# Kernel tuning notes

Measured on AMD Instinct MI355X. Metric: run time of the kernel, lower is better.

The kernel has to match this reference:

```python
import jax, jax.numpy as jnp
import numpy as np

B, N, NODE_DIM, D, H, K, VP = 64, 1024, 8, 128, 4, 16, 128
FF = 512


def _layernorm(x, g, b):
    m = jnp.mean(x, axis=-1, keepdims=True)
    v = jnp.var(x, axis=-1, keepdims=True)
    return (x - m) * jax.lax.rsqrt(v + 1e-5) * g + b


def setup_inputs() -> dict:
    key = jax.random.key(0)
    kit = iter(jax.random.split(key, 64))

    def w(*shape):
        fan_in = shape[-2] if len(shape) >= 2 else shape[-1]
        return jax.random.normal(next(kit), shape, jnp.float32) / np.sqrt(fan_in)

    return dict(
        node_inputs=jax.random.normal(next(kit), (B, N, NODE_DIM), jnp.float32),
        node_padding_mask=jnp.zeros((B, 1, N), jnp.bool_),
        current_index=jax.random.randint(next(kit), (B, 1, 1), 0, N),
        viewpoints=jax.random.randint(next(kit), (B, VP, 1), 0, N),
        viewpoint_padding_mask=jnp.zeros((B, 1, VP), jnp.bool_),
        adj_list=jax.random.randint(next(kit), (B, N, K), 0, N),
        W_init=w(NODE_DIM, D), b_init=jnp.zeros((D,), jnp.float32),
        gcn_W=w(4, D, D), gcn_b=jnp.zeros((4, D), jnp.float32),
        tc_fc_W=w(D, D), tc_fc_b=jnp.zeros((D,), jnp.float32),
        tc_ln1_g=jnp.ones((D,), jnp.float32), tc_ln1_b=jnp.zeros((D,), jnp.float32),
        Wq=w(D, H * D), bq=jnp.zeros((H * D,), jnp.float32),
        Wk=w(D, H * D), bk=jnp.zeros((H * D,), jnp.float32),
        Wv=w(D, H * D), bv=jnp.zeros((H * D,), jnp.float32),
        tc_ln2_g=jnp.ones((D,), jnp.float32), tc_ln2_b=jnp.zeros((D,), jnp.float32),
        sg_fc_W=w(D, D), sg_fc_b=jnp.zeros((D,), jnp.float32),
        dec_Wq=w(D, D), dec_Wk=w(D, D), dec_Wv=w(D, D), dec_Wo=w(D, D),
        dec_ln1_g=jnp.ones((D,), jnp.float32), dec_ln1_b=jnp.zeros((D,), jnp.float32),
        ff_W1=w(D, FF), ff_b1=jnp.zeros((FF,), jnp.float32),
        ff_W2=w(FF, D), ff_b2=jnp.zeros((D,), jnp.float32),
        dec_ln2_g=jnp.ones((D,), jnp.float32), dec_ln2_b=jnp.zeros((D,), jnp.float32),
        q_W=w(3 * D, 1), q_b=jnp.zeros((1,), jnp.float32),
    )


def _forward(node_inputs, node_padding_mask, current_index, viewpoints, viewpoint_padding_mask, adj_list,
             W_init, b_init, gcn_W, gcn_b, tc_fc_W, tc_fc_b, tc_ln1_g, tc_ln1_b,
             Wq, bq, Wk, bk, Wv, bv, tc_ln2_g, tc_ln2_b, sg_fc_W, sg_fc_b,
             dec_Wq, dec_Wk, dec_Wv, dec_Wo, dec_ln1_g, dec_ln1_b,
             ff_W1, ff_b1, ff_W2, ff_b2, dec_ln2_g, dec_ln2_b, q_W, q_b):
    Bb, Nn, nd = node_inputs.shape
    d = W_init.shape[1]
    nH = Wq.shape[1] // d  # SGFormer attention heads (per-head dim = d)
    BN = Bb * Nn
    # ---- initial embedding + batched block-diagonal sparse edges (prepare_batch_data) ----
    x0 = node_inputs.reshape(BN, nd) @ W_init + b_init
    offset = (jnp.arange(Bb) * Nn)[:, None, None]
    valid = adj_list >= 0
    row = (jnp.broadcast_to(jnp.arange(Nn)[None, :, None], adj_list.shape) + offset).reshape(-1)
    col = (jnp.where(valid, adj_list, 0) + offset).reshape(-1)
    ew = valid.reshape(-1).astype(x0.dtype)
    deg = jax.ops.segment_sum(ew, row, num_segments=BN) + 1.0  # +1 self-loop
    dinv = jax.lax.rsqrt(deg)
    enorm = (dinv[row] * dinv[col] * ew)[:, None]

    def gcn_conv(h, W, b):
        hw = h @ W
        agg = jax.ops.segment_sum(enorm * hw[col], row, num_segments=BN)
        return agg + hw / deg[:, None] + b  # self-loop term D^-1 * x W

    h = x0
    n_layers = gcn_W.shape[0]
    for i in range(n_layers):
        h = gcn_conv(h, gcn_W[i], gcn_b[i])
        if i < n_layers - 1:
            h = jax.nn.relu(h)
    gnn_out = h
    # ---- SGFormer TransConv: fc -> LN -> relu, then linear global attention over all BN nodes ----
    z0 = jax.nn.relu(_layernorm(x0 @ tc_fc_W + tc_fc_b, tc_ln1_g, tc_ln1_b))
    q = (z0 @ Wq + bq).reshape(BN, nH, d)
    k = (z0 @ Wk + bk).reshape(BN, nH, d)
    v = (z0 @ Wv + bv).reshape(BN, nH, d)
    qs = q / jnp.linalg.norm(q)  # global Frobenius norm, as in SGFormer
    ks = k / jnp.linalg.norm(k)
    Nf = jnp.asarray(BN, x0.dtype)
    kvs = jnp.einsum('lhm,lhd->hmd', ks, v)
    num = jnp.einsum('nhm,hmd->nhd', qs, kvs) + Nf * v
    den = jnp.einsum('nhm,hm->nh', qs, ks.sum(axis=0))[..., None] + Nf
    attn = (num / den).mean(axis=1)  # mean over heads -> [BN, d]
    z = jax.nn.relu(_layernorm(0.5 * attn + 0.5 * z0, tc_ln2_g, tc_ln2_b))  # alpha=0.5 residual
    enhanced = ((0.8 * gnn_out + 0.2 * z) @ sg_fc_W + sg_fc_b).reshape(Bb, Nn, d)  # graph_weight=0.8
    # ---- decoder: gather current node, masked cross-attention to all nodes ----
    cur = jnp.take_along_axis(enhanced, jnp.broadcast_to(current_index, (Bb, 1, d)), axis=1)
    dH = 4
    dk = d // dH
    qd = (cur @ dec_Wq).reshape(Bb, 1, dH, dk).transpose(0, 2, 1, 3)
    kd = (enhanced @ dec_Wk).reshape(Bb, Nn, dH, dk).transpose(0, 2, 1, 3)
    vd = (enhanced @ dec_Wv).reshape(Bb, Nn, dH, dk).transpose(0, 2, 1, 3)
    scores = jnp.einsum('bhqe,bhne->bhqn', qd, kd) / np.sqrt(dk).astype(np.float32)
    scores = jnp.where(node_padding_mask[:, None, :, :], -1e9, scores)
    wts = jax.nn.softmax(scores, axis=-1)
    att = jnp.einsum('bhqn,bhne->bhqe', wts, vd).transpose(0, 2, 1, 3).reshape(Bb, 1, d) @ dec_Wo
    t = _layernorm(cur + att, dec_ln1_g, dec_ln1_b)
    glob = _layernorm(t + jax.nn.relu(t @ ff_W1 + ff_b1) @ ff_W2 + ff_b2, dec_ln2_g, dec_ln2_b)
    # ---- Q head: gather viewpoints, concat(global, current, viewpoint) -> Linear(3d, 1) ----
    Vp = viewpoints.shape[1]
    vp = jnp.take_along_axis(enhanced, jnp.broadcast_to(viewpoints, (Bb, Vp, d)), axis=1)
    cs = jnp.concatenate([glob, cur], axis=-1)  # [B,1,2d]
    af = jnp.concatenate([jnp.broadcast_to(cs, (Bb, Vp, 2 * d)), vp], axis=-1)
    return af @ q_W + q_b  # [B, Vp, 1]


def reference(node_inputs, node_padding_mask, current_index, viewpoints, viewpoint_padding_mask, adj_list,
              W_init, b_init, gcn_W, gcn_b, tc_fc_W, tc_fc_b, tc_ln1_g, tc_ln1_b,
              Wq, bq, Wk, bk, Wv, bv, tc_ln2_g, tc_ln2_b, sg_fc_W, sg_fc_b,
              dec_Wq, dec_Wk, dec_Wv, dec_Wo, dec_ln1_g, dec_ln1_b,
              ff_W1, ff_b1, ff_W2, ff_b2, dec_ln2_g, dec_ln2_b, q_W, q_b):
    return _forward(node_inputs, node_padding_mask, current_index, viewpoints, viewpoint_padding_mask, adj_list,
                    W_init, b_init, gcn_W, gcn_b, tc_fc_W, tc_fc_b, tc_ln1_g, tc_ln1_b,
                    Wq, bq, Wk, bk, Wv, bv, tc_ln2_g, tc_ln2_b, sg_fc_W, sg_fc_b,
                    dec_Wq, dec_Wk, dec_Wv, dec_Wo, dec_ln1_g, dec_ln1_b,
                    ff_W1, ff_b1, ff_W2, ff_b2, dec_ln2_g, dec_ln2_b, q_W, q_b)
```

## Files before the change

### kernel.cpp

```cpp
#include <hip/hip_runtime.h>

#define BNn 65536L

typedef unsigned short u16;
typedef unsigned int u32;
typedef __attribute__((ext_vector_type(8))) short short8;
typedef __attribute__((ext_vector_type(4))) float f32x4;

__device__ inline u16 f2b(float f){ u32 u = __float_as_uint(f); u32 r = (u + 0x7fffu + ((u>>16)&1u))>>16; return (u16)r; }
__device__ inline float b2f(u16 b){ return __uint_as_float(((u32)b)<<16); }

__global__ __launch_bounds__(256) void k_init(const float* __restrict__ gcnW, const float* __restrict__ tcW,
                       const float* __restrict__ sgW, const float* __restrict__ dKW,
                       const float* __restrict__ dVW,
                       const float* __restrict__ Wq, const float* __restrict__ Wk, const float* __restrict__ Wv,
                       const float* __restrict__ in, const float* __restrict__ Wi, const float* __restrict__ bi,
                       const int* __restrict__ adj, float* __restrict__ dinv,
                       u16* __restrict__ wts, float* __restrict__ SqSkz, u16* __restrict__ x0) {
  __shared__ u16 sT[64 * 136];
  __shared__ float Ws[1024];
  __shared__ float bs[128];
  __shared__ float ins[256];
  int bid = blockIdx.x, t = threadIdx.x;
  if (bid < 41) {
    if (bid == 40) {
      if (t < 130) SqSkz[t] = 0.0f;
      return;
    }
    const float* src; long dst; int lds_src;
    if (bid < 16) {
      int mtx = bid >> 1, kh = bid & 1;
      src = (mtx < 4 ? gcnW + mtx * 16384 : mtx == 4 ? tcW : mtx == 5 ? sgW : mtx == 6 ? dKW : dVW) + kh * 64 * 128;
      dst = (long)mtx * 16384 + kh * 64;
      lds_src = 128;
    } else {
      int q = bid - 16; int mat = q >> 3, rem = q & 7, kh = rem >> 2, cb = rem & 3;
      src = (mat == 0 ? Wq : mat == 1 ? Wk : Wv) + kh * 64 * 512 + cb * 128;
      dst = 131072L + (long)(mat * 512 + cb * 128) * 128 + kh * 64;
      lds_src = 512;
    }
#pragma unroll
    for (int i = 0; i < 32; i++) {
      int idx = t + i * 256; int row = idx >> 7, col = idx & 127;
      sT[row * 136 + col] = f2b(src[(long)row * lds_src + col]);
    }
    __syncthreads();
    {
      int n = t >> 1, kb = t & 1;
      u16 ob[32];
#pragma unroll
      for (int k = 0; k < 32; k++) ob[k] = sT[(kb * 32 + k) * 136 + n];
      uint4* o4 = (uint4*)(wts + dst + (long)n * 128 + kb * 32);
      uint4* s4 = (uint4*)ob;
#pragma unroll
      for (int k = 0; k < 4; k++) o4[k] = s4[k];
    }
    return;
  }
  int b = bid - 41;
  long row0 = (long)b * 32;
  if (b < 256) {
    int n = b * 256 + t;
    int cnt = 0;
#pragma unroll
    for (int j = 0; j < 16; j++) cnt += (adj[(long)n * 16 + j] >= 0) ? 1 : 0;
    dinv[n] = rsqrtf((float)cnt + 1.0f);
  }
#pragma unroll
  for (int i = 0; i < 4; i++) Ws[t + i * 256] = Wi[t + i * 256];
  if (t < 128) bs[t] = bi[t];
  ins[t] = in[row0 * 8 + t];
  __syncthreads();
  int row = t >> 3, seg = t & 7;
  float acc[16];
#pragma unroll
  for (int i = 0; i < 16; i++) acc[i] = bs[seg * 16 + i];
#pragma unroll
  for (int k = 0; k < 8; k++) {
    float f = ins[row * 8 + k];
#pragma unroll
    for (int i = 0; i < 16; i++) acc[i] += f * Ws[k * 128 + seg * 16 + i];
  }
  u16 ob[16];
#pragma unroll
  for (int i = 0; i < 16; i++) ob[i] = f2b(acc[i]);
  uint4* o4 = (uint4*)(x0 + (row0 + row) * 128 + seg * 16);
  uint4* s4 = (uint4*)ob;
  o4[0] = s4[0]; o4[1] = s4[1];
}

template<int EPI>
__global__ __launch_bounds__(256) void k_gemm(const u16* __restrict__ A,
                                              const u16* __restrict__ WT,
                                              const float* __restrict__ bias,
                                              const float* __restrict__ lng,
                                              const float* __restrict__ lnb,
                                              u16* __restrict__ C,
                                              u16* __restrict__ CT) {
  __shared__ u16 sW[128 * 136];
  int t = threadIdx.x;
  long row0 = (long)blockIdx.x * 128;
  int wave = t >> 6, lane = t & 63, m = lane & 15, g = lane >> 4;
#pragma unroll
  for (int i = 0; i < 8; i++) {
    int idx = t + i * 256; int row = idx >> 4, ch = idx & 15;
    *(float4*)(sW + row * 136 + ch * 8) = *(const float4*)(WT + row * 128 + ch * 8);
  }
  short8 a[2][4];
#pragma unroll
  for (int i = 0; i < 2; i++) {
    const u16* aG = A + (row0 + wave * 32 + i * 16 + m) * 128 + g * 8;
#pragma unroll
    for (int s = 0; s < 4; s++) a[i][s] = *(const short8*)(aG + s * 32);
  }
  __syncthreads();
  f32x4 acc[2][8];
#pragma unroll
  for (int i = 0; i < 2; i++)
#pragma unroll
    for (int c = 0; c < 8; c++) acc[i][c] = (f32x4){0.f, 0.f, 0.f, 0.f};
#pragma unroll
  for (int s = 0; s < 4; s++) {
#pragma unroll
    for (int c = 0; c < 8; c++) {
      short8 bb = *(const short8*)(sW + (c * 16 + m) * 136 + g * 8 + s * 32);
      acc[0][c] = __builtin_amdgcn_mfma_f32_16x16x32_bf16(a[0][s], bb, acc[0][c], 0, 0, 0);
      acc[1][c] = __builtin_amdgcn_mfma_f32_16x16x32_bf16(a[1][s], bb, acc[1][c], 0, 0, 0);
    }
  }
#pragma unroll
  for (int c = 0; c < 8; c++) {
    float bc = bias ? bias[c * 16 + m] : 0.0f;
#pragma unroll
    for (int i = 0; i < 2; i++)
#pragma unroll
      for (int r = 0; r < 4; r++) acc[i][c][r] += bc;
  }
  if (EPI == 2) {
    float gg[8], bb2[8];
#pragma unroll
    for (int c = 0; c < 8; c++) { gg[c] = lng[c * 16 + m]; bb2[c] = lnb[c * 16 + m]; }
#pragma unroll
    for (int i = 0; i < 2; i++)
#pragma unroll
      for (int r = 0; r < 4; r++) {
        float s1 = 0.f, s2 = 0.f;
#pragma unroll
        for (int c = 0; c < 8; c++) { float y = acc[i][c][r]; s1 += y; s2 += y * y; }
#pragma unroll
        for (int mask = 1; mask < 16; mask <<= 1) { s1 += __shfl_xor(s1, mask); s2 += __shfl_xor(s2, mask); }
        float mu = s1 * (1.f / 128.f);
        float rstd = rsqrtf(s2 * (1.f / 128.f) - mu * mu + 1e-5f);
#pragma unroll
        for (int c = 0; c < 8; c++)
          acc[i][c][r] = fmaxf((acc[i][c][r] - mu) * rstd * gg[c] + bb2[c], 0.f);
      }
  }
#pragma unroll
  for (int i = 0; i < 2; i++) {
    long rb = row0 + wave * 32 + i * 16 + g * 4;
#pragma unroll
    for (int c = 0; c < 8; c++) {
      int col = c * 16 + m;
      u16 ob[4];
#pragma unroll
      for (int r = 0; r < 4; r++) {
        float y = acc[i][c][r];
        if (EPI == 1) y = fmaxf(y, 0.f);
        ob[r] = f2b(y);
        C[(rb + r) * 128 + col] = ob[r];
      }
      if (CT) {
        uint2 p;
        p.x = ((u32)ob[1] << 16) | ob[0]; p.y = ((u32)ob[3] << 16) | ob[2];
        *(uint2*)(CT + (long)col * BNn + rb) = p;
      }
    }
  }
}

__global__ __launch_bounds__(256) void k_gcn(const u16* __restrict__ h,
                                             const u16* __restrict__ WT,
                                             const int* __restrict__ adj,
                                             const float* __restrict__ dinv,
                                             const float* __restrict__ gb,
                                             u16* __restrict__ out, int relu) {
  __shared__ u16 sA[64 * 132];
  __shared__ u16 sW[128 * 132];
  int t = threadIdx.x;
  int lane = t & 63;
  int p = blockIdx.x;
  long n0 = ((long)(p & 63) << 10) + ((long)(p >> 6) << 6);
#pragma unroll
  for (int i = 0; i < 8; i++) {
    int idx = t + i * 256; int row = idx >> 4, ch = idx & 15;
    *(float4*)(sW + row * 132 + ch * 8) = *(const float4*)(WT + row * 128 + ch * 8);
  }
  {
    int row = t >> 2, seg = t & 3;
    long n = n0 + row;
    float din = dinv[n];
    float d2v = din * din;
    int4 a4 = *(const int4*)(adj + n * 16 + seg * 4);
    int cols[4]; float enq[4];
    int bb = ((int)(n >> 10)) << 10;
    const int* ap = &a4.x;
#pragma unroll
    for (int q = 0; q < 4; q++) {
      int a = ap[q];
      int valid = a >= 0;
      int cc = (valid ? a : 0) + bb;
      cols[q] = cc;
      enq[q] = valid ? din * dinv[cc] : 0.0f;
    }
    float acc[32];
    {
      const u16* hr = h + n * 128 + seg * 32;
      uint4 v0 = *(const uint4*)(hr), v1 = *(const uint4*)(hr + 8), v2 = *(const uint4*)(hr + 16), v3 = *(const uint4*)(hr + 24);
      const u16* pv = (const u16*)&v0;
#pragma unroll
      for (int i = 0; i < 8; i++) acc[i] = b2f(pv[i]) * d2v;
      pv = (const u16*)&v1;
#pragma unroll
      for (int i = 0; i < 8; i++) acc[8 + i] = b2f(pv[i]) * d2v;
      pv = (const u16*)&v2;
#pragma unroll
      for (int i = 0; i < 8; i++) acc[16 + i] = b2f(pv[i]) * d2v;
      pv = (const u16*)&v3;
#pragma unroll
      for (int i = 0; i < 8; i++) acc[24 + i] = b2f(pv[i]) * d2v;
    }
#pragma unroll
    for (int jb = 0; jb < 4; jb++) {
      int cc4[4]; float e4[4];
      uint4 nv[16];
#pragma unroll
      for (int q = 0; q < 4; q++) {
        int j = jb * 4 + q;
        int src = (lane & 60) | (j >> 2);
        cc4[q] = __shfl(cols[j & 3], src);
        e4[q] = __shfl(enq[j & 3], src);
        const u16* nb = h + (long)cc4[q] * 128 + seg * 32;
        nv[q * 4 + 0] = *(const uint4*)(nb);
        nv[q * 4 + 1] = *(const uint4*)(nb + 8);
        nv[q * 4 + 2] = *(const uint4*)(nb + 16);
        nv[q * 4 + 3] = *(const uint4*)(nb + 24);
      }
#pragma unroll
      for (int q = 0; q < 4; q++) {
        float e = e4[q];
#pragma unroll
        for (int v = 0; v < 4; v++) {
          const u16* pv = (const u16*)&nv[q * 4 + v];
#pragma unroll
          for (int i = 0; i < 8; i++) acc[v * 8 + i] += e * b2f(pv[i]);
        }
      }
    }
    u16 ob[32];
#pragma unroll
    for (int i = 0; i < 32; i++) ob[i] = f2b(acc[i]);
    uint4* o4 = (uint4*)(sA + row * 132 + seg * 32);
    uint4* s4 = (uint4*)ob;
#pragma unroll
    for (int i = 0; i < 4; i++) o4[i] = s4[i];
  }
  __syncthreads();
  int wave = t >> 6, m = lane & 15, g = lane >> 4;
  const u16* aB = sA + (wave * 16 + m) * 132 + g * 8;
  short8 a[4];
#pragma unroll
  for (int s = 0; s < 4; s++) a[s] = *(const short8*)(aB + s * 32);
  f32x4 acc[8];
#pragma unroll
  for (int c = 0; c < 8; c++) {
    float bc = gb[c * 16 + m];
    acc[c] = (f32x4){bc, bc, bc, bc};
  }
#pragma unroll
  for (int s = 0; s < 4; s++) {
#pragma unroll
    for (int c = 0; c < 8; c++) {
      short8 bb = *(const short8*)(sW + (c * 16 + m) * 132 + g * 8 + s * 32);
      acc[c] = __builtin_amdgcn_mfma_f32_16x16x32_bf16(a[s], bb, acc[c], 0, 0, 0);
    }
  }
#pragma unroll
  for (int c = 0; c < 8; c++) {
    int col = c * 16 + m;
#pragma unroll
    for (int r = 0; r < 4; r++) {
      float y = acc[c][r];
      if (relu) y = fmaxf(y, 0.f);
      out[(n0 + wave * 16 + g * 4 + r) * 128 + col] = f2b(y);
    }
  }
}

__global__ __launch_bounds__(256) void k_gram(const u16* __restrict__ z0T,
                                              float* __restrict__ Gpart, float* __restrict__ zsum) {
  __shared__ u16 sZT[128 * 264];
  int t = threadIdx.x;
  int wave = t >> 6, lane = t & 63, m = lane & 15, g = lane >> 4;
  f32x4 acc[2][8];
#pragma unroll
  for (int i = 0; i < 2; i++)
#pragma unroll
    for (int c = 0; c < 8; c++) acc[i][c] = (f32x4){0.f, 0.f, 0.f, 0.f};
  float zs = 0.f;
  for (int sl = 0; sl < 2; sl++) {
    long k0 = (long)(blockIdx.x * 2 + sl) * 256;
    __syncthreads();
#pragma unroll
    for (int i = 0; i < 16; i++) {
      int idx = t + i * 256; int mm = idx >> 5, ch = idx & 31;
      *(float4*)(sZT + mm * 264 + ch * 8) = *(const float4*)(z0T + (long)mm * BNn + k0 + ch * 8);
    }
    __syncthreads();
#pragma unroll
    for (int kk = 0; kk < 8; kk++) {
      short8 a0 = *(const short8*)(sZT + (wave * 32 + m) * 264 + kk * 32 + g * 8);
      short8 a1 = *(const short8*)(sZT + (wave * 32 + 16 + m) * 264 + kk * 32 + g * 8);
#pragma unroll
      for (int c = 0; c < 8; c++) {
        short8 bb = *(const short8*)(sZT + (c * 16 + m) * 264 + kk * 32 + g * 8);
        acc[0][c] = __builtin_amdgcn_mfma_f32_16x16x32_bf16(a0, bb, acc[0][c], 0, 0, 0);
        acc[1][c] = __builtin_amdgcn_mfma_f32_16x16x32_bf16(a1, bb, acc[1][c], 0, 0, 0);
      }
    }
    if (t < 128) {
      float s = 0.f;
      for (int j = 0; j < 256; j++) s += b2f(sZT[t * 264 + j]);
      zs += s;
    }
  }
  if (t < 128) atomicAdd(&zsum[t], zs);
  float* P = Gpart + (long)blockIdx.x * 16384 + wave * 4096;
#pragma unroll
  for (int i = 0; i < 2; i++)
#pragma unroll
    for (int c = 0; c < 8; c++)
      *(f32x4*)(P + (i * 8 + c) * 256 + lane * 4) = acc[i][c];
}

__global__ void k_gram_red(const float* __restrict__ Gpart, float* __restrict__ G) {
  int o = blockIdx.x * 256 + threadIdx.x;
  float s = 0.f;
  for (int b = 0; b < 128; b++) s += Gpart[(long)b * 16384 + o];
  int wave = o >> 12, rem = o & 4095;
  int ic = rem >> 8, i = ic >> 3, c = ic & 7;
  int rem2 = rem & 255, lane = rem2 >> 2, q = rem2 & 3;
  int m = lane & 15, g = lane >> 4;
  int mi = wave * 32 + i * 16 + g * 4 + q;
  int mj = c * 16 + m;
  G[mi * 128 + mj] = s;
}

__global__ __launch_bounds__(256) void k_statskvs(const float* __restrict__ Wq, const float* __restrict__ bq,
                                                  const float* __restrict__ Wk, const float* __restrict__ bk,
                                                  const float* __restrict__ Wv, const float* __restrict__ bv,
                                                  const float* __restrict__ G, const float* __restrict__ zsum,
                                                  float* __restrict__ ksum,
                                                  float* __restrict__ Sq, float* __restrict__ Sk,
                                                  u16* __restrict__ kvsT) {
  int t = threadIdx.x;
  int blk = blockIdx.x;
  if (blk < 2) {
    int c = blk * 256 + t;
    float s = 0.f;
    for (int i = 0; i < 128; i++) s += Wk[i * 512 + c] * zsum[i];
    ksum[c] = s + 65536.0f * bk[c];
    return;
  }
  if (blk < 130) {
    __shared__ float wcol[128];
    __shared__ float red[256];
    int bi = blk - 2;
    int isK = bi >> 6;
    const float* W = isK ? Wk : Wq;
    const float* bb = isK ? bk : bq;
    float* S = isK ? Sk : Sq;
    int c0 = (bi & 63) * 8;
    float tot = 0.f;
    for (int cc = 0; cc < 8; cc++) {
      int c = c0 + cc;
      __syncthreads();
      if (t < 128) wcol[t] = W[t * 512 + c];
      __syncthreads();
      float v = 0.f;
      if (t < 128) {
        float uu = 0.f;
        for (int j = 0; j < 128; j++) uu += G[t * 128 + j] * wcol[j];
        v = uu * wcol[t] + 2.0f * bb[c] * wcol[t] * zsum[t];
      }
      red[t] = v;
      __syncthreads();
      for (int o = 128; o > 0; o >>= 1) { if (t < o) red[t] += red[t + o]; __syncthreads(); }
      if (t == 0) tot += red[0] + 65536.0f * bb[c] * bb[c];
    }
    if (t == 0) atomicAdd(S, tot);
    return;
  }
  {
    __shared__ float wv8[128][8];
    __shared__ float U[128][8];
    __shared__ float zv[8];
    int bi = blk - 130;
    int h = bi >> 4, dg = bi & 15;
    if (t < 128) {
#pragma unroll
      for (int dd = 0; dd < 8; dd++) wv8[t][dd] = Wv[t * 512 + h * 128 + dg * 8 + dd];
    }
    __syncthreads();
    {
      int i = t & 127, du = t >> 7;
      float a0 = 0.f, a1 = 0.f, a2 = 0.f, a3 = 0.f;
      for (int j = 0; j < 128; j++) {
        float gg = G[i * 128 + j];
        a0 += gg * wv8[j][du * 4 + 0]; a1 += gg * wv8[j][du * 4 + 1];
        a2 += gg * wv8[j][du * 4 + 2]; a3 += gg * wv8[j][du * 4 + 3];
      }
      U[i][du * 4 + 0] = a0; U[i][du * 4 + 1] = a1; U[i][du * 4 + 2] = a2; U[i][du * 4 + 3] = a3;
    }
    if (t < 8) {
      float s = 0.f;
      for (int i = 0; i < 128; i++) s += zsum[i] * wv8[i][t];
      zv[t] = s;
    }
    __syncthreads();
    {
      int m = t & 127, du = t >> 7;
      int colk = h * 128 + m;
      float bkm = bk[colk];
      float a[4] = {0.f, 0.f, 0.f, 0.f};
      float wkzs = 0.f;
      for (int i = 0; i < 128; i++) {
        float wk = Wk[i * 512 + colk];
        wkzs += wk * zsum[i];
#pragma unroll
        for (int q = 0; q < 4; q++) a[q] += wk * U[i][du * 4 + q];
      }
#pragma unroll
      for (int q = 0; q < 4; q++) {
        int dd = du * 4 + q;
        int cold = h * 128 + dg * 8 + dd;
        float val = a[q] + wkzs * bv[cold] + bkm * zv[dd] + 65536.0f * bkm * bv[cold];
        kvsT[h * 16384 + (dg * 8 + dd) * 128 + m] = f2b(val);
      }
    }
  }
}

__global__ __launch_bounds__(256) void k_prepB(const float* __restrict__ Wq, const float* __restrict__ bq,
                                               const float* __restrict__ Wv, const float* __restrict__ bv,
                                               const u16* __restrict__ kvsT, const float* __restrict__ ksum,
                                               const float* __restrict__ SqSk,
                                               u16* __restrict__ Bmat, float* __restrict__ cAv,
                                               u16* __restrict__ U16, float* __restrict__ consts) {
  __shared__ float kvr[8][128];
  int t = threadIdx.x;
  int h = blockIdx.x >> 4, dg = blockIdx.x & 15;
  float inv = rsqrtf(SqSk[0] * SqSk[1]);
  for (int i = t; i < 1024; i += 256) {
    int dl = i >> 7, m = i & 127;
    kvr[dl][m] = b2f(kvsT[h * 16384 + (dg * 8 + dl) * 128 + m]);
  }
  __syncthreads();
  {
    int k = t & 127, du = t >> 7;
    const float* wqr = Wq + k * 512 + h * 128;
    float acc[4] = {0.f, 0.f, 0.f, 0.f};
    for (int m = 0; m < 128; m++) {
      float w = wqr[m];
#pragma unroll
      for (int q = 0; q < 4; q++) acc[q] += w * kvr[du * 4 + q][m];
    }
#pragma unroll
    for (int q = 0; q < 4; q++) {
      int dd = dg * 8 + du * 4 + q;
      float mv = acc[q] * inv + 65536.0f * Wv[k * 512 + h * 128 + dd];
      Bmat[((long)h * 128 + dd) * 128 + k] = f2b(mv);
    }
  }
  if (t < 8) {
    float s = 0.f;
    for (int m = 0; m < 128; m++) s += bq[h * 128 + m] * kvr[t][m];
    cAv[h * 128 + dg * 8 + t] = s * inv + 65536.0f * bv[h * 128 + dg * 8 + t];
  }
  if (dg == 0) {
    if (t < 128) {
      float s = 0.f;
      for (int m = 0; m < 128; m++) s += Wq[t * 512 + h * 128 + m] * ksum[h * 128 + m];
      U16[h * 128 + t] = f2b(s * inv);
    } else if (t == 128) {
      float s = 0.f;
      for (int m = 0; m < 128; m++) s += bq[h * 128 + m] * ksum[h * 128 + m];
      consts[h] = s * inv + 65536.0f;
    }
    if (h == 0) {
      for (int i = t; i < 1536; i += 256) U16[512 + i] = 0;
    }
  }
}

__global__ __launch_bounds__(256, 2) void k_numfuse(const u16* __restrict__ z0, const u16* __restrict__ gnn,
                                                 const u16* __restrict__ Bmat,
                                                 const float* __restrict__ cAv, const u16* __restrict__ U16,
                                                 const float* __restrict__ consts,
                                                 const float* __restrict__ g2, const float* __restrict__ b2,
                                                 const u16* __restrict__ wsg, const float* __restrict__ sgb,
                                                 u16* __restrict__ enh) {
  __shared__ u16 sA[128 * 132];
  __shared__ u16 sB[128 * 132];
  __shared__ float rden[512];
  __shared__ float caL[512];
  int t = threadIdx.x;
  long n0 = (long)blockIdx.x * 128;
  int wave = t >> 6, lane = t & 63, m = lane & 15, g = lane >> 4;
  u16* myA = sA + wave * 32 * 132;
  {
    const u16* zg = z0 + (n0 + wave * 32) * 128;
#pragma unroll
    for (int i = 0; i < 8; i++) {
      int idx = lane + i * 64;
      *(float4*)(myA + idx * 8 + (idx >> 4) * 4) = *(const float4*)(zg + idx * 8);
    }
  }
  caL[t] = cAv[t]; caL[t + 256] = cAv[t + 256];
  const u16* aB = sA + (wave * 32 + m) * 132 + g * 8;
  short8 a[2][4];
#pragma unroll
  for (int i = 0; i < 2; i++)
#pragma unroll
    for (int s = 0; s < 4; s++) a[i][s] = *(const short8*)(aB + i * 16 * 132 + s * 32);
  {
    f32x4 accd0 = (f32x4){0.f, 0.f, 0.f, 0.f}, accd1 = (f32x4){0.f, 0.f, 0.f, 0.f};
#pragma unroll
    for (int s = 0; s < 4; s++) {
      short8 ub = *(const short8*)(U16 + m * 128 + g * 8 + s * 32);
      accd0 = __builtin_amdgcn_mfma_f32_16x16x32_bf16(a[0][s], ub, accd0, 0, 0, 0);
      accd1 = __builtin_amdgcn_mfma_f32_16x16x32_bf16(a[1][s], ub, accd1, 0, 0, 0);
    }
    if (m < 4) {
      float ch = consts[m];
#pragma unroll
      for (int r = 0; r < 4; r++) {
        rden[(wave * 32 + g * 4 + r) * 4 + m] = 1.0f / (accd0[r] + ch);
        rden[(wave * 32 + 16 + g * 4 + r) * 4 + m] = 1.0f / (accd1[r] + ch);
      }
    }
  }
  f32x4 attn[2][8];
#pragma unroll
  for (int i = 0; i < 2; i++)
#pragma unroll
    for (int c = 0; c < 8; c++) attn[i][c] = (f32x4){0.f, 0.f, 0.f, 0.f};
  for (int h = 0; h < 4; h++) {
    __syncthreads();
    {
      const u16* src = Bmat + (long)h * 16384;
#pragma unroll
      for (int i = 0; i < 8; i++) {
        int idx = t + i * 256;
        *(float4*)(sB + idx * 8 + (idx >> 4) * 4) = *(const float4*)(src + idx * 8);
      }
    }
    __syncthreads();
    f32x4 acc[2][8];
#pragma unroll
    for (int c = 0; c < 8; c++) {
      float ca = caL[h * 128 + c * 16 + m];
      acc[0][c] = (f32x4){ca, ca, ca, ca};
      acc[1][c] = (f32x4){ca, ca, ca, ca};
    }
#pragma unroll
    for (int s = 0; s < 4; s++) {
#pragma unroll
      for (int c = 0; c < 8; c++) {
        short8 bb = *(const short8*)(sB + (c * 16 + m) * 132 + g * 8 + s * 32);
        acc[0][c] = __builtin_amdgcn_mfma_f32_16x16x32_bf16(a[0][s], bb, acc[0][c], 0, 0, 0);
        acc[1][c] = __builtin_amdgcn_mfma_f32_16x16x32_bf16(a[1][s], bb, acc[1][c], 0, 0, 0);
      }
    }
    float rd0[4], rd1[4];
#pragma unroll
    for (int r = 0; r < 4; r++) {
      rd0[r] = rden[(wave * 32 + g * 4 + r) * 4 + h];
      rd1[r] = rden[(wave * 32 + 16 + g * 4 + r) * 4 + h];
    }
#pragma unroll
    for (int c = 0; c < 8; c++)
#pragma unroll
      for (int r = 0; r < 4; r++) {
        attn[0][c][r] += acc[0][c][r] * rd0[r];
        attn[1][c][r] += acc[1][c][r] * rd1[r];
      }
  }
  float4 gv[8];
  {
    const u16* gg = gnn + (n0 + wave * 32) * 128;
#pragma unroll
    for (int i = 0; i < 8; i++) {
      int idx = lane + i * 64;
      gv[i] = *(const float4*)(gg + idx * 8);
    }
  }
  float y[2][8][4];
#pragma unroll
  for (int i = 0; i < 2; i++)
#pragma unroll
    for (int c = 0; c < 8; c++)
#pragma unroll
      for (int r = 0; r < 4; r++)
        y[i][c][r] = 0.125f * attn[i][c][r] + 0.5f * b2f(sA[(wave * 32 + i * 16 + g * 4 + r) * 132 + c * 16 + m]);
  float mu[2][4], rstd[2][4];
#pragma unroll
  for (int i = 0; i < 2; i++)
#pragma unroll
    for (int r = 0; r < 4; r++) {
      float s1 = 0.f, s2 = 0.f;
#pragma unroll
      for (int c = 0; c < 8; c++) { float v = y[i][c][r]; s1 += v; s2 += v * v; }
#pragma unroll
      for (int mask = 1; mask < 16; mask <<= 1) { s1 += __shfl_xor(s1, mask); s2 += __shfl_xor(s2, mask); }
      float mm2 = s1 * (1.f / 128.f);
      mu[i][r] = mm2; rstd[i][r] = rsqrtf(s2 * (1.f / 128.f) - mm2 * mm2 + 1e-5f);
    }
#pragma unroll
  for (int i = 0; i < 8; i++) {
    int idx = lane + i * 64;
    *(float4*)(myA + idx * 8 + (idx >> 4) * 4) = gv[i];
  }
#pragma unroll
  for (int c = 0; c < 8; c++) {
    int d = c * 16 + m;
    float ggc = g2[d], bbc = b2[d];
#pragma unroll
    for (int i = 0; i < 2; i++)
#pragma unroll
      for (int r = 0; r < 4; r++) {
        int loc = (wave * 32 + i * 16 + g * 4 + r) * 132 + d;
        float zr = fmaxf((y[i][c][r] - mu[i][r]) * rstd[i][r] * ggc + bbc, 0.f);
        sA[loc] = f2b(0.8f * b2f(sA[loc]) + 0.2f * zr);
      }
  }
  __syncthreads();
  {
#pragma unroll
    for (int i = 0; i < 8; i++) {
      int idx = t + i * 256;
      *(float4*)(sB + idx * 8 + (idx >> 4) * 4) = *(const float4*)(wsg + idx * 8);
    }
  }
  __syncthreads();
  short8 ap[2][4];
#pragma unroll
  for (int i = 0; i < 2; i++)
#pragma unroll
    for (int s = 0; s < 4; s++) ap[i][s] = *(const short8*)(aB + i * 16 * 132 + s * 32);
  f32x4 acc2[2][8];
#pragma unroll
  for (int c = 0; c < 8; c++) {
    float bc = sgb[c * 16 + m];
    acc2[0][c] = (f32x4){bc, bc, bc, bc};
    acc2[1][c] = (f32x4){bc, bc, bc, bc};
  }
#pragma unroll
  for (int s = 0; s < 4; s++) {
#pragma unroll
    for (int c = 0; c < 8; c++) {
      short8 bb = *(const short8*)(sB + (c * 16 + m) * 132 + g * 8 + s * 32);
      acc2[0][c] = __builtin_amdgcn_mfma_f32_16x16x32_bf16(ap[0][s], bb, acc2[0][c], 0, 0, 0);
      acc2[1][c] = __builtin_amdgcn_mfma_f32_16x16x32_bf16(ap[1][s], bb, acc2[1][c], 0, 0, 0);
    }
  }
#pragma unroll
  for (int i = 0; i < 2; i++)
#pragma unroll
    for (int c = 0; c < 8; c++) {
      int d = c * 16 + m;
#pragma unroll
      for (int r = 0; r < 4; r++)
        enh[(n0 + wave * 32 + i * 16 + g * 4 + r) * 128 + d] = f2b(acc2[i][c][r]);
    }
}

__global__ __launch_bounds__(1024) void k_dec(const u16* __restrict__ enh, const int* __restrict__ cidx,
                                             const int* __restrict__ vps,
                                             const float* __restrict__ dWq, const float* __restrict__ dWk,
                                             const float* __restrict__ dWv, const float* __restrict__ dWo,
                                             const float* __restrict__ ln1g, const float* __restrict__ ln1b,
                                             const float* __restrict__ fW1, const float* __restrict__ fb1,
                                             const float* __restrict__ fW2, const float* __restrict__ fb2,
                                             const float* __restrict__ ln2g, const float* __restrict__ ln2b,
                                             const float* __restrict__ qW, const float* __restrict__ qb,
                                             float* __restrict__ out) {
  __shared__ float cur[128], qd[128], qtL[4][128];
  __shared__ float scL[4][1024];
  __shared__ float mxs[4], dinvs[4];
  __shared__ float pvL[16][4][128];
  __shared__ float sH[4][128];
  __shared__ float att[128], tn[128], tv[128], f1[512], glob[128];
  __shared__ float red[16], red2[16];
  __shared__ float mu_s, rs_s, base_s;
  int b = blockIdx.x, t = threadIdx.x;
  int wave = t >> 6, lane = t & 63;
  const u16* eb = enh + (long)b * 1024 * 128;
  if (t < 128) cur[t] = b2f(eb[(long)cidx[b] * 128 + t]);
  __syncthreads();
  {
    int o = t >> 3, p = t & 7;
    float s = 0.f;
    int k0 = p * 16;
#pragma unroll
    for (int k = 0; k < 16; k++) s += cur[k0 + k] * dWq[(k0 + k) * 128 + o];
    s += __shfl_xor(s, 1); s += __shfl_xor(s, 2); s += __shfl_xor(s, 4);
    if (p == 0) qd[o] = s;
  }
  __syncthreads();
  if (t < 512) {
    int h = t >> 7, col = t & 127;
    float s = 0.f;
#pragma unroll
    for (int c = 0; c < 32; c++) s += dWk[col * 128 + h * 32 + c] * qd[h * 32 + c];
    qtL[h][col] = s;
  }
  __syncthreads();
  const float scale = 0.17677669529663687f;
  {
    const u16* er = eb + (long)t * 128;
    float s0 = 0.f, s1 = 0.f, s2 = 0.f, s3 = 0.f;
#pragma unroll
    for (int i8 = 0; i8 < 16; i8++) {
      short8 ev = *(const short8*)(er + i8 * 8);
#pragma unroll
      for (int j = 0; j < 8; j++) {
        float e = b2f((u16)ev[j]);
        int k = i8 * 8 + j;
        s0 += e * qtL[0][k]; s1 += e * qtL[1][k]; s2 += e * qtL[2][k]; s3 += e * qtL[3][k];
      }
    }
    scL[0][t] = s0 * scale; scL[1][t] = s1 * scale; scL[2][t] = s2 * scale; scL[3][t] = s3 * scale;
  }
  __syncthreads();
  if (wave < 4) {
    float mx = -3.0e38f;
    for (int k = lane; k < 1024; k += 64) mx = fmaxf(mx, scL[wave][k]);
#pragma unroll
    for (int msk = 1; msk < 64; msk <<= 1) mx = fmaxf(mx, __shfl_xor(mx, msk));
    if (lane == 0) mxs[wave] = mx;
  }
  __syncthreads();
  {
    int h = t >> 8, i4 = (t & 255) * 4;
    f32x4 v = *(f32x4*)&scL[h][i4];
    float mv = mxs[h];
    v[0] = __expf(v[0] - mv); v[1] = __expf(v[1] - mv); v[2] = __expf(v[2] - mv); v[3] = __expf(v[3] - mv);
    *(f32x4*)&scL[h][i4] = v;
  }
  __syncthreads();
  if (wave < 4) {
    float sm = 0.f;
    for (int k = lane; k < 1024; k += 64) sm += scL[wave][k];
#pragma unroll
    for (int msk = 1; msk < 64; msk <<= 1) sm += __shfl_xor(sm, msk);
    if (lane == 0) dinvs[wave] = 1.0f / sm;
  }
  __syncthreads();
  {
    int seg = t & 15, part = t >> 4;
    float acc[4][8];
#pragma unroll
    for (int h = 0; h < 4; h++)
#pragma unroll
      for (int j = 0; j < 8; j++) acc[h][j] = 0.f;
    for (int i = 0; i < 16; i++) {
      int n = part * 16 + i;
      short8 e8 = *(const short8*)(eb + (long)n * 128 + seg * 8);
      float p0 = scL[0][n], p1 = scL[1][n], p2 = scL[2][n], p3 = scL[3][n];
#pragma unroll
      for (int j = 0; j < 8; j++) {
        float e = b2f((u16)e8[j]);
        acc[0][j] += p0 * e; acc[1][j] += p1 * e; acc[2][j] += p2 * e; acc[3][j] += p3 * e;
      }
    }
#pragma unroll
    for (int h = 0; h < 4; h++)
#pragma unroll
      for (int j = 0; j < 8; j++) {
        acc[h][j] += __shfl_xor(acc[h][j], 16);
        acc[h][j] += __shfl_xor(acc[h][j], 32);
      }
    if (lane < 16) {
#pragma unroll
      for (int h = 0; h < 4; h++)
#pragma unroll
        for (int j = 0; j < 8; j++) pvL[wave][h][seg * 8 + j] = acc[h][j];
    }
  }
  __syncthreads();
  if (t < 512) {
    int h = t >> 7, d = t & 127;
    float s = 0.f;
#pragma unroll
    for (int w = 0; w < 16; w++) s += pvL[w][h][d];
    sH[h][d] = s;
  }
  __syncthreads();
  {
    int o = t >> 3, p = t & 7;
    int h = o >> 5, e = o & 31;
    float s = 0.f;
    int k0 = p * 16;
#pragma unroll
    for (int k = 0; k < 16; k++) s += sH[h][k0 + k] * dWv[(k0 + k) * 128 + h * 32 + e];
    s += __shfl_xor(s, 1); s += __shfl_xor(s, 2); s += __shfl_xor(s, 4);
    if (p == 0) att[o] = s * dinvs[h];
  }
  __syncthreads();
  {
    int o = t >> 3, p = t & 7;
    float s = 0.f;
    int k0 = p * 16;
#pragma unroll
    for (int k = 0; k < 16; k++) s += att[k0 + k] * dWo[(k0 + k) * 128 + o];
    s += __shfl_xor(s, 1); s += __shfl_xor(s, 2); s += __shfl_xor(s, 4);
    if (p == 0) tv[o] = cur[o] + s;
  }
  __syncthreads();
  {
    float v = (t < 128) ? tv[t] : 0.f;
    float s1 = v, s2 = v * v;
#pragma unroll
    for (int msk = 1; msk < 64; msk <<= 1) { s1 += __shfl_xor(s1, msk); s2 += __shfl_xor(s2, msk); }
    if (lane == 0) { red[wave] = s1; red2[wave] = s2; }
  }
  __syncthreads();
  if (t == 0) {
    float s1 = 0.f, s2 = 0.f;
#pragma unroll
    for (int w = 0; w < 16; w++) { s1 += red[w]; s2 += red2[w]; }
    float mm = s1 / 128.0f;
    mu_s = mm; rs_s = rsqrtf(s2 / 128.0f - mm * mm + 1e-5f);
  }
  __syncthreads();
  if (t < 128) tn[t] = (tv[t] - mu_s) * rs_s * ln1g[t] + ln1b[t];
  __syncthreads();
  if (t < 512) {
    float s = fb1[t];
    for (int k = 0; k < 128; k++) s += tn[k] * fW1[k * 512 + t];
    f1[t] = fmaxf(s, 0.0f);
  }
  __syncthreads();
  {
    int o = t >> 3, p = t & 7;
    float s = 0.f;
    int k0 = p * 64;
#pragma unroll
    for (int k = 0; k < 64; k++) s += f1[k0 + k] * fW2[(k0 + k) * 128 + o];
    s += __shfl_xor(s, 1); s += __shfl_xor(s, 2); s += __shfl_xor(s, 4);
    if (p == 0) tv[o] = tn[o] + s + fb2[o];
  }
  __syncthreads();
  {
    float v = (t < 128) ? tv[t] : 0.f;
    float s1 = v, s2 = v * v;
#pragma unroll
    for (int msk = 1; msk < 64; msk <<= 1) { s1 += __shfl_xor(s1, msk); s2 += __shfl_xor(s2, msk); }
    if (lane == 0) { red[wave] = s1; red2[wave] = s2; }
  }
  __syncthreads();
  if (t == 0) {
    float s1 = 0.f, s2 = 0.f;
#pragma unroll
    for (int w = 0; w < 16; w++) { s1 += red[w]; s2 += red2[w]; }
    float mm = s1 / 128.0f;
    mu_s = mm; rs_s = rsqrtf(s2 / 128.0f - mm * mm + 1e-5f);
  }
  __syncthreads();
  if (t < 128) glob[t] = (tv[t] - mu_s) * rs_s * ln2g[t] + ln2b[t];
  __syncthreads();
  {
    float v = 0.f;
    if (t < 256) v = (t < 128 ? glob[t] : cur[t - 128]) * qW[t];
    float s = v;
#pragma unroll
    for (int msk = 1; msk < 64; msk <<= 1) s += __shfl_xor(s, msk);
    if (lane == 0) red[wave] = s;
  }
  __syncthreads();
  if (t == 0) {
    float s = 0.f;
#pragma unroll
    for (int w = 0; w < 16; w++) s += red[w];
    base_s = s + qb[0];
  }
  __syncthreads();
  {
    int o = t >> 3, p = t & 7;
    int vi = vps[b * 128 + o];
    const u16* er = eb + (long)vi * 128 + p * 16;
    short8 e0 = *(const short8*)(er);
    short8 e1 = *(const short8*)(er + 8);
    float s = 0.f;
#pragma unroll
    for (int j = 0; j < 8; j++) {
      s += b2f((u16)e0[j]) * qW[256 + p * 16 + j];
      s += b2f((u16)e1[j]) * qW[256 + p * 16 + 8 + j];
    }
    s += __shfl_xor(s, 1); s += __shfl_xor(s, 2); s += __shfl_xor(s, 4);
    if (p == 0) out[b * 128 + o] = base_s + s;
  }
}

extern "C" void kernel_launch(void* const* d_in, const int* in_sizes, int n_in,
                              void* d_out, int out_size, void* d_ws, size_t ws_size,
                              hipStream_t stream) {
  const float* node_in = (const float*)d_in[0];
  const int* cur_idx   = (const int*)d_in[2];
  const int* vps       = (const int*)d_in[3];
  const int* adj       = (const int*)d_in[5];
  const float* W_init  = (const float*)d_in[6];
  const float* b_init  = (const float*)d_in[7];
  const float* gcn_W   = (const float*)d_in[8];
  const float* gcn_b   = (const float*)d_in[9];
  const float* tc_fc_W = (const float*)d_in[10];
  const float* tc_fc_b = (const float*)d_in[11];
  const float* ln1g    = (const float*)d_in[12];
  const float* ln1b    = (const float*)d_in[13];
  const float* Wq      = (const float*)d_in[14];
  const float* bq      = (const float*)d_in[15];
  const float* Wk      = (const float*)d_in[16];
  const float* bk      = (const float*)d_in[17];
  const float* Wv      = (const float*)d_in[18];
  const float* bv      = (const float*)d_in[19];
  const float* ln2g    = (const float*)d_in[20];
  const float* ln2b    = (const float*)d_in[21];
  const float* sg_W    = (const float*)d_in[22];
  const float* sg_b    = (const float*)d_in[23];
  const float* dWq     = (const float*)d_in[24];
  const float* dWk     = (const float*)d_in[25];
  const float* dWv     = (const float*)d_in[26];
  const float* dWo     = (const float*)d_in[27];
  const float* dln1g   = (const float*)d_in[28];
  const float* dln1b   = (const float*)d_in[29];
  const float* fW1     = (const float*)d_in[30];
  const float* fb1     = (const float*)d_in[31];
  const float* fW2     = (const float*)d_in[32];
  const float* fb2     = (const float*)d_in[33];
  const float* dln2g   = (const float*)d_in[34];
  const float* dln2b   = (const float*)d_in[35];
  const float* qW      = (const float*)d_in[36];
  const float* qb      = (const float*)d_in[37];

  char* base = (char*)d_ws;
  u16* bufA = (u16*)base;
  u16* bufB = (u16*)(base + 16777216);
  u16* bufC = (u16*)(base + 33554432);
  u16* z0T  = (u16*)(base + 50331648);
  float* Gpart = (float*)(base + 67108864);
  char* sm = base + 83886080;
  u16* kvsT   = (u16*)sm;
  u16* wts    = (u16*)(sm + 131072);
  float* bqkv = (float*)(sm + 131072 + 655360);
  float* ksum = bqkv + 1536;
  float* SqSk = ksum + 512;
  float* zsum = SqSk + 2;
  float* Gm   = zsum + 128;
  float* dinv = Gm + 16384;
  float* cAv  = dinv + BNn;
  float* consts = cAv + 512;
  u16* Bmat = (u16*)(consts + 4);
  u16* U16m = Bmat + 65536;

  k_init<<<2089, 256, 0, stream>>>(gcn_W, tc_fc_W, sg_W, dWk, dWv, Wq, Wk, Wv,
                                   node_in, W_init, b_init, adj, dinv, wts, SqSk, bufA);

  k_gemm<2><<<512, 256, 0, stream>>>(bufA, wts + 4 * 16384, tc_fc_b, ln1g, ln1b, bufB, z0T);

  k_gram<<<128, 256, 0, stream>>>(z0T, Gpart, zsum);
  k_gram_red<<<64, 256, 0, stream>>>(Gpart, Gm);
  k_statskvs<<<194, 256, 0, stream>>>(Wq, bq, Wk, bk, Wv, bv, Gm, zsum, ksum, SqSk, SqSk + 1, kvsT);
  k_prepB<<<64, 256, 0, stream>>>(Wq, bq, Wv, bv, kvsT, ksum, SqSk, Bmat, cAv, U16m, consts);

  k_gcn<<<1024, 256, 0, stream>>>(bufA, wts + 0 * 16384, adj, dinv, gcn_b + 0, bufC, 1);
  k_gcn<<<1024, 256, 0, stream>>>(bufC, wts + 1 * 16384, adj, dinv, gcn_b + 128, bufA, 1);
  k_gcn<<<1024, 256, 0, stream>>>(bufA, wts + 2 * 16384, adj, dinv, gcn_b + 256, bufC, 1);
  k_gcn<<<1024, 256, 0, stream>>>(bufC, wts + 3 * 16384, adj, dinv, gcn_b + 384, bufA, 0);

  k_numfuse<<<512, 256, 0, stream>>>(bufB, bufA, Bmat, cAv, U16m, consts, ln2g, ln2b,
                                     wts + 5 * 16384, sg_b, bufB);

  k_dec<<<64, 1024, 0, stream>>>(bufB, cur_idx, vps, dWq, dWk, dWv, dWo, dln1g, dln1b,
                                 fW1, fb1, fW2, fb2, dln2g, dln2b, qW, qb, (float*)d_out);
}
```

Baseline: 441.7 us.

## Collapse decoder tail into single-wave phases to remove block barriers

```diff
diff --git a/kernel.cpp b/kernel.cpp
--- a/kernel.cpp
+++ b/kernel.cpp
@@ -695,35 +695,41 @@
                                              const float* __restrict__ ln2g, const float* __restrict__ ln2b,
                                              const float* __restrict__ qW, const float* __restrict__ qb,
                                              float* __restrict__ out) {
-  __shared__ float cur[128], qd[128], qtL[4][128];
+  __shared__ float qtL[4][128];
   __shared__ float scL[4][1024];
-  __shared__ float mxs[4], dinvs[4];
+  __shared__ float dinvs[4];
   __shared__ float pvL[16][4][128];
   __shared__ float sH[4][128];
-  __shared__ float att[128], tn[128], tv[128], f1[512], glob[128];
-  __shared__ float red[16], red2[16];
-  __shared__ float mu_s, rs_s, base_s;
+  __shared__ float att[128], tn[128], f1[512];
   int b = blockIdx.x, t = threadIdx.x;
   int wave = t >> 6, lane = t & 63;
   const u16* eb = enh + (long)b * 1024 * 128;
-  if (t < 128) cur[t] = b2f(eb[(long)cidx[b] * 128 + t]);
-  __syncthreads();
-  {
-    int o = t >> 3, p = t & 7;
-    float s = 0.f;
-    int k0 = p * 16;
-#pragma unroll
-    for (int k = 0; k < 16; k++) s += cur[k0 + k] * dWq[(k0 + k) * 128 + o];
-    s += __shfl_xor(s, 1); s += __shfl_xor(s, 2); s += __shfl_xor(s, 4);
-    if (p == 0) qd[o] = s;
-  }
-  __syncthreads();
-  if (t < 512) {
-    int h = t >> 7, col = t & 127;
-    float s = 0.f;
-#pragma unroll
-    for (int c = 0; c < 32; c++) s += dWk[col * 128 + h * 32 + c] * qd[h * 32 + c];
-    qtL[h][col] = s;
+  float curr0 = 0.f, curr1 = 0.f;
+  if (wave == 0) {
+    int ci = cidx[b];
+    const u16* cr = eb + (long)ci * 128;
+    curr0 = b2f(cr[lane]);
+    curr1 = b2f(cr[lane + 64]);
+    float qd0 = 0.f, qd1 = 0.f;
+#pragma unroll 16
+    for (int k = 0; k < 128; k++) {
+      float ck = __shfl((k < 64) ? curr0 : curr1, k & 63);
+      qd0 += ck * dWq[k * 128 + lane];
+      qd1 += ck * dWq[k * 128 + lane + 64];
+    }
+#pragma unroll
+    for (int h = 0; h < 4; h++) {
+      float s0 = 0.f, s1 = 0.f;
+#pragma unroll
+      for (int c = 0; c < 32; c++) {
+        int idx = h * 32 + c;
+        float qv = __shfl((idx < 64) ? qd0 : qd1, idx & 63);
+        s0 += dWk[lane * 128 + idx] * qv;
+        s1 += dWk[(lane + 64) * 128 + idx] * qv;
+      }
+      qtL[h][lane] = s0;
+      qtL[h][lane + 64] = s1;
+    }
   }
   __syncthreads();
   const float scale = 0.17677669529663687f;
@@ -744,24 +750,15 @@
   }
   __syncthreads();
   if (wave < 4) {
+    float v[16];
     float mx = -3.0e38f;
-    for (int k = lane; k < 1024; k += 64) mx = fmaxf(mx, scL[wave][k]);
+#pragma unroll
+    for (int i = 0; i < 16; i++) { v[i] = scL[wave][lane + i * 64]; mx = fmaxf(mx, v[i]); }
 #pragma unroll
     for (int msk = 1; msk < 64; msk <<= 1) mx = fmaxf(mx, __shfl_xor(mx, msk));
-    if (lane == 0) mxs[wave] = mx;
-  }
-  __syncthreads();
-  {
-    int h = t >> 8, i4 = (t & 255) * 4;
-    f32x4 v = *(f32x4*)&scL[h][i4];
-    float mv = mxs[h];
-    v[0] = __expf(v[0] - mv); v[1] = __expf(v[1] - mv); v[2] = __expf(v[2] - mv); v[3] = __expf(v[3] - mv);
-    *(f32x4*)&scL[h][i4] = v;
-  }
-  __syncthreads();
-  if (wave < 4) {
     float sm = 0.f;
-    for (int k = lane; k < 1024; k += 64) sm += scL[wave][k];
+#pragma unroll
+    for (int i = 0; i < 16; i++) { float e = __expf(v[i] - mx); scL[wave][lane + i * 64] = e; sm += e; }
 #pragma unroll
     for (int msk = 1; msk < 64; msk <<= 1) sm += __shfl_xor(sm, msk);
     if (lane == 0) dinvs[wave] = 1.0f / sm;
@@ -799,117 +796,101 @@
     }
   }
   __syncthreads();
-  if (t < 512) {
-    int h = t >> 7, d = t & 127;
-    float s = 0.f;
-#pragma unroll
-    for (int w = 0; w < 16; w++) s += pvL[w][h][d];
-    sH[h][d] = s;
-  }
-  __syncthreads();
-  {
-    int o = t >> 3, p = t & 7;
+  if (wave != 0) return;
+#pragma unroll
+  for (int h = 0; h < 4; h++)
+#pragma unroll
+    for (int d2 = 0; d2 < 2; d2++) {
+      int d = d2 * 64 + lane;
+      float s = 0.f;
+#pragma unroll
+      for (int w = 0; w < 16; w++) s += pvL[w][h][d];
+      sH[h][d] = s;
+    }
+#pragma unroll
+  for (int o2 = 0; o2 < 2; o2++) {
+    int o = o2 * 64 + lane;
     int h = o >> 5, e = o & 31;
     float s = 0.f;
-    int k0 = p * 16;
-#pragma unroll
-    for (int k = 0; k < 16; k++) s += sH[h][k0 + k] * dWv[(k0 + k) * 128 + h * 32 + e];
-    s += __shfl_xor(s, 1); s += __shfl_xor(s, 2); s += __shfl_xor(s, 4);
-    if (p == 0) att[o] = s * dinvs[h];
-  }
-  __syncthreads();
-  {
-    int o = t >> 3, p = t & 7;
+    for (int k = 0; k < 128; k++) s += sH[h][k] * dWv[k * 128 + h * 32 + e];
+    att[o] = s * dinvs[h];
+  }
+  float tvr[2];
+#pragma unroll
+  for (int o2 = 0; o2 < 2; o2++) {
+    int o = o2 * 64 + lane;
     float s = 0.f;
-    int k0 = p * 16;
-#pragma unroll
-    for (int k = 0; k < 16; k++) s += att[k0 + k] * dWo[(k0 + k) * 128 + o];
-    s += __shfl_xor(s, 1); s += __shfl_xor(s, 2); s += __shfl_xor(s, 4);
-    if (p == 0) tv[o] = cur[o] + s;
-  }
-  __syncthreads();
-  {
-    float v = (t < 128) ? tv[t] : 0.f;
-    float s1 = v, s2 = v * v;
+    for (int k = 0; k < 128; k++) s += att[k] * dWo[k * 128 + o];
+    tvr[o2] = (o2 == 0 ? curr0 : curr1) + s;
+  }
+  {
+    float s1 = tvr[0] + tvr[1], s2 = tvr[0] * tvr[0] + tvr[1] * tvr[1];
 #pragma unroll
     for (int msk = 1; msk < 64; msk <<= 1) { s1 += __shfl_xor(s1, msk); s2 += __shfl_xor(s2, msk); }
-    if (lane == 0) { red[wave] = s1; red2[wave] = s2; }
-  }
-  __syncthreads();
-  if (t == 0) {
-    float s1 = 0.f, s2 = 0.f;
-#pragma unroll
-    for (int w = 0; w < 16; w++) { s1 += red[w]; s2 += red2[w]; }
-    float mm = s1 / 128.0f;
-    mu_s = mm; rs_s = rsqrtf(s2 / 128.0f - mm * mm + 1e-5f);
-  }
-  __syncthreads();
-  if (t < 128) tn[t] = (tv[t] - mu_s) * rs_s * ln1g[t] + ln1b[t];
-  __syncthreads();
-  if (t < 512) {
-    float s = fb1[t];
-    for (int k = 0; k < 128; k++) s += tn[k] * fW1[k * 512 + t];
-    f1[t] = fmaxf(s, 0.0f);
-  }
-  __syncthreads();
-  {
-    int o = t >> 3, p = t & 7;
+    float mm = s1 * (1.f / 128.f);
+    float rs = rsqrtf(s2 * (1.f / 128.f) - mm * mm + 1e-5f);
+#pragma unroll
+    for (int o2 = 0; o2 < 2; o2++) {
+      int o = o2 * 64 + lane;
+      tn[o] = (tvr[o2] - mm) * rs * ln1g[o] + ln1b[o];
+    }
+  }
+  {
+    float sacc[8];
+    int c0 = lane * 8;
+#pragma unroll
+    for (int j = 0; j < 8; j++) sacc[j] = fb1[c0 + j];
+    for (int k = 0; k < 128; k++) {
+      float tk = tn[k];
+      float4 w0 = *(const float4*)(fW1 + k * 512 + c0);
+      float4 w1 = *(const float4*)(fW1 + k * 512 + c0 + 4);
+      sacc[0] += tk * w0.x; sacc[1] += tk * w0.y; sacc[2] += tk * w0.z; sacc[3] += tk * w0.w;
+      sacc[4] += tk * w1.x; sacc[5] += tk * w1.y; sacc[6] += tk * w1.z; sacc[7] += tk * w1.w;
+    }
+#pragma unroll
+    for (int j = 0; j < 8; j++) f1[c0 + j] = fmaxf(sacc[j], 0.0f);
+  }
+  float glb[2];
+  {
+    float s0 = 0.f, s1 = 0.f;
+    int o0 = lane * 2;
+    for (int k = 0; k < 512; k++) {
+      float fk = f1[k];
+      float2 w = *(const float2*)(fW2 + k * 128 + o0);
+      s0 += fk * w.x; s1 += fk * w.y;
+    }
+    float tv20 = tn[o0] + s0 + fb2[o0];
+    float tv21 = tn[o0 + 1] + s1 + fb2[o0 + 1];
+    float s1r = tv20 + tv21, s2r = tv20 * tv20 + tv21 * tv21;
+#pragma unroll
+    for (int msk = 1; msk < 64; msk <<= 1) { s1r += __shfl_xor(s1r, msk); s2r += __shfl_xor(s2r, msk); }
+    float mm = s1r * (1.f / 128.f);
+    float rs = rsqrtf(s2r * (1.f / 128.f) - mm * mm + 1e-5f);
+    glb[0] = (tv20 - mm) * rs * ln2g[o0] + ln2b[o0];
+    glb[1] = (tv21 - mm) * rs * ln2g[o0 + 1] + ln2b[o0 + 1];
+  }
+  float base;
+  {
+    int o0 = lane * 2;
+    float p = glb[0] * qW[o0] + glb[1] * qW[o0 + 1]
+            + curr0 * qW[128 + lane] + curr1 * qW[128 + lane + 64];
+#pragma unroll
+    for (int msk = 1; msk < 64; msk <<= 1) p += __shfl_xor(p, msk);
+    base = p + qb[0];
+  }
+#pragma unroll
+  for (int o2 = 0; o2 < 2; o2++) {
+    int o = lane * 2 + o2;
+    int vi = vps[b * 128 + o];
+    const u16* er = eb + (long)vi * 128;
     float s = 0.f;
-    int k0 = p * 64;
-#pragma unroll
-    for (int k = 0; k < 64; k++) s += f1[k0 + k] * fW2[(k0 + k) * 128 + o];
-    s += __shfl_xor(s, 1); s += __shfl_xor(s, 2); s += __shfl_xor(s, 4);
-    if (p == 0) tv[o] = tn[o] + s + fb2[o];
-  }
-  __syncthreads();
-  {
-    float v = (t < 128) ? tv[t] : 0.f;
-    float s1 = v, s2 = v * v;
-#pragma unroll
-    for (int msk = 1; msk < 64; msk <<= 1) { s1 += __shfl_xor(s1, msk); s2 += __shfl_xor(s2, msk); }
-    if (lane == 0) { red[wave] = s1; red2[wave] = s2; }
-  }
-  __syncthreads();
-  if (t == 0) {
-    float s1 = 0.f, s2 = 0.f;
-#pragma unroll
-    for (int w = 0; w < 16; w++) { s1 += red[w]; s2 += red2[w]; }
-    float mm = s1 / 128.0f;
-    mu_s = mm; rs_s = rsqrtf(s2 / 128.0f - mm * mm + 1e-5f);
-  }
-  __syncthreads();
-  if (t < 128) glob[t] = (tv[t] - mu_s) * rs_s * ln2g[t] + ln2b[t];
-  __syncthreads();
-  {
-    float v = 0.f;
-    if (t < 256) v = (t < 128 ? glob[t] : cur[t - 128]) * qW[t];
-    float s = v;
-#pragma unroll
-    for (int msk = 1; msk < 64; msk <<= 1) s += __shfl_xor(s, msk);
-    if (lane == 0) red[wave] = s;
-  }
-  __syncthreads();
-  if (t == 0) {
-    float s = 0.f;
-#pragma unroll
-    for (int w = 0; w < 16; w++) s += red[w];
-    base_s = s + qb[0];
-  }
-  __syncthreads();
-  {
-    int o = t >> 3, p = t & 7;
-    int vi = vps[b * 128 + o];
-    const u16* er = eb + (long)vi * 128 + p * 16;
-    short8 e0 = *(const short8*)(er);
-    short8 e1 = *(const short8*)(er + 8);
-    float s = 0.f;
-#pragma unroll
-    for (int j = 0; j < 8; j++) {
-      s += b2f((u16)e0[j]) * qW[256 + p * 16 + j];
-      s += b2f((u16)e1[j]) * qW[256 + p * 16 + 8 + j];
-    }
-    s += __shfl_xor(s, 1); s += __shfl_xor(s, 2); s += __shfl_xor(s, 4);
-    if (p == 0) out[b * 128 + o] = base_s + s;
+#pragma unroll
+    for (int i8 = 0; i8 < 16; i8++) {
+      short8 ev = *(const short8*)(er + i8 * 8);
+#pragma unroll
+      for (int j = 0; j < 8; j++) s += b2f((u16)ev[j]) * qW[256 + i8 * 8 + j];
+    }
+    out[b * 128 + o] = base + s;
   }
 }
 
```

After: 443.6 us. No clear change (+0.4%).
